# Kernel optimization log

Hardware: AMD Instinct MI355X
Metric: run time of the kernel (lower is better)

## Reference

```python
import jax, jax.numpy as jnp
import numpy as np

N, IN_DIM, HID, OUT_DIM, H = 4096, 256, 256, 256, 2
E_RAND = 131072
BN_EPS = 1e-5


def _bn(h, gamma, beta):
    # BatchNorm1d training-mode math: batch mean, biased variance
    mu = jnp.mean(h, axis=0)
    var = jnp.var(h, axis=0)
    return (h - mu) * jax.lax.rsqrt(var + BN_EPS) * gamma + beta


def setup_inputs() -> dict:
    key = jax.random.key(0)
    ks = jax.random.split(key, 16)
    x = jax.random.normal(ks[0], (N, IN_DIM), jnp.float32)
    # random edges + self loops (self loops guarantee every row has >=1 neighbor)
    rnd = jax.random.randint(ks[1], (2, E_RAND), 0, N, jnp.int64)
    loops = jnp.stack([jnp.arange(N, dtype=jnp.int64)] * 2)
    edge_index = jnp.concatenate([rnd, loops], axis=1)
    s = 1.0 / np.sqrt(IN_DIM)
    sh = 1.0 / np.sqrt(HID)
    return {
        "x": x,
        "edge_index": edge_index,
        "wq": jax.random.uniform(ks[2], (IN_DIM, HID), jnp.float32, -s, s),
        "bq": jnp.zeros((HID,), jnp.float32),
        "wk": jax.random.uniform(ks[3], (IN_DIM, HID), jnp.float32, -s, s),
        "bk": jnp.zeros((HID,), jnp.float32),
        "wv": jax.random.uniform(ks[4], (IN_DIM, HID), jnp.float32, -s, s),
        "bv": jnp.zeros((HID,), jnp.float32),
        "wo": jax.random.uniform(ks[5], (HID, IN_DIM), jnp.float32, -sh, sh),
        "bo": jnp.zeros((IN_DIM,), jnp.float32),
        "eps": jnp.zeros((1, 1), jnp.float32),
        "w1": jax.random.uniform(ks[6], (IN_DIM, HID), jnp.float32, -s, s),
        "b1": jnp.zeros((HID,), jnp.float32),
        "g1": jnp.ones((HID,), jnp.float32),
        "be1": jnp.zeros((HID,), jnp.float32),
        "w2": jax.random.uniform(ks[7], (HID, OUT_DIM), jnp.float32, -sh, sh),
        "b2": jnp.zeros((OUT_DIM,), jnp.float32),
        "g2": jnp.ones((OUT_DIM,), jnp.float32),
        "be2": jnp.zeros((OUT_DIM,), jnp.float32),
    }


def reference(x, edge_index, wq, bq, wk, bk, wv, bv, wo, bo, eps,
              w1, b1, g1, be1, w2, b2, g2, be2):
    n = x.shape[0]
    hd = HID // H
    q = (x @ wq + bq).reshape(n, H, hd)
    k = (x @ wk + bk).reshape(n, H, hd)
    v = (x @ wv + bv).reshape(n, H, hd)
    scores = jnp.einsum('nhd,mhd->nhm', q, k) / (hd ** 0.5)  # [n,H,n]
    row, col = edge_index[0], edge_index[1]
    mask = jnp.zeros((n, H, n), bool).at[row, :, col].set(True)
    scores = jnp.where(mask, scores, -jnp.inf)
    attn = jax.nn.softmax(scores, axis=-1)
    v_agg = jnp.einsum('nhm,mhd->nhd', attn, v).reshape(n, HID)
    v_agg = v_agg @ wo + bo + eps * x
    h = jax.nn.relu(_bn(v_agg @ w1 + b1, g1, be1))
    h = jax.nn.relu(_bn(h @ w2 + b2, g2, be2))
    return h  # dropout is identity (eval)
```

## Files before the change

kernel.cpp:

```cpp
#include <hip/hip_runtime.h>
#include <math.h>

#define N_NODES 4096
#define DIM 256
#define GK 256
#define MWORDS 128
#define MAXNBR 192

typedef float f32x4 __attribute__((ext_vector_type(4)));
typedef short s16x8 __attribute__((ext_vector_type(8)));
typedef short s16x4 __attribute__((ext_vector_type(4)));

__device__ __forceinline__ unsigned short bf16_rne(float f) {
  unsigned int u = __float_as_uint(f);
  u += 0x7FFFu + ((u >> 16) & 1u);
  return (unsigned short)(u >> 16);
}

__device__ __forceinline__ void split_bf16(float f, short& hi, short& lo) {
  unsigned short h = bf16_rne(f);
  float hf = __uint_as_float(((unsigned int)h) << 16);
  hi = (short)h;
  lo = (short)bf16_rne(f - hf);
}

__device__ __forceinline__ int swz(int row, int col) {
  return row * 64 + (col ^ ((row & 7) << 3));
}

template <int EPI, bool PRESPLIT, bool WRITE_C, bool SPLIT_OUT, bool STATS_OUT>
__device__ __forceinline__ void gemm_core(
    short* As_hi, short* As_lo, short* Bs_hi, short* Bs_lo, float* red,
    const float* bnsc, const float* bnsh,
    const float* __restrict__ Af, const short* __restrict__ A_hi,
    const short* __restrict__ A_lo,
    const short* __restrict__ Wt_hi, const short* __restrict__ Wt_lo,
    const float* __restrict__ bias, float* __restrict__ C, int ldc,
    short* __restrict__ C_hi, short* __restrict__ C_lo,
    int m0, int n0, const float* __restrict__ X, float ev,
    float* __restrict__ osum, float* __restrict__ osq) {
  const int tid = threadIdx.x;
  const int lane = tid & 63;
  const int wave = tid >> 6;
  const int wr = wave >> 1, wc = wave & 1;
  const int l15 = lane & 15;
  const int lg = lane >> 4;

  f32x4 acc[2][2] = {};

  for (int kt = 0; kt < GK; kt += 64) {
    __syncthreads();
    if (PRESPLIT) {
#pragma unroll
      for (int i = 0; i < 2; ++i) {
        const int row = (tid >> 3) + i * 32;
        const int kc = (tid & 7) * 8;
        const size_t g = (size_t)(m0 + row) * GK + kt + kc;
        s16x8 ah = *(const s16x8*)(A_hi + g);
        s16x8 al = *(const s16x8*)(A_lo + g);
        const int o = swz(row, kc);
        *(s16x8*)&As_hi[o] = ah;
        *(s16x8*)&As_lo[o] = al;
      }
    } else {
#pragma unroll
      for (int i = 0; i < 4; ++i) {
        const int row = (tid >> 4) + i * 16;
        const int kc = (tid & 15) * 4;
        float4 av = *(const float4*)(Af + (size_t)(m0 + row) * GK + kt + kc);
        if (EPI == 2) {
          const float4 s4 = *(const float4*)&bnsc[kt + kc];
          const float4 h4 = *(const float4*)&bnsh[kt + kc];
          av.x = fmaxf(fmaf(av.x, s4.x, h4.x), 0.f);
          av.y = fmaxf(fmaf(av.y, s4.y, h4.y), 0.f);
          av.z = fmaxf(fmaf(av.z, s4.z, h4.z), 0.f);
          av.w = fmaxf(fmaf(av.w, s4.w, h4.w), 0.f);
        }
        short h0, l0, h1, l1, h2, l2, h3, l3;
        split_bf16(av.x, h0, l0);
        split_bf16(av.y, h1, l1);
        split_bf16(av.z, h2, l2);
        split_bf16(av.w, h3, l3);
        s16x4 hv = {h0, h1, h2, h3};
        s16x4 lv = {l0, l1, l2, l3};
        const int o = swz(row, kc);
        *(s16x4*)&As_hi[o] = hv;
        *(s16x4*)&As_lo[o] = lv;
      }
    }
#pragma unroll
    for (int i = 0; i < 2; ++i) {
      const int row = (tid >> 3) + i * 32;
      const int kc = (tid & 7) * 8;
      const size_t g = (size_t)(n0 + row) * GK + kt + kc;
      s16x8 bh = *(const s16x8*)(Wt_hi + g);
      s16x8 bl = *(const s16x8*)(Wt_lo + g);
      const int o = swz(row, kc);
      *(s16x8*)&Bs_hi[o] = bh;
      *(s16x8*)&Bs_lo[o] = bl;
    }
    __syncthreads();
#pragma unroll
    for (int kk = 0; kk < 2; ++kk) {
      s16x8 ah[2], al[2], bh[2], bl[2];
#pragma unroll
      for (int f = 0; f < 2; ++f) {
        const int ao = swz(wr * 32 + f * 16 + l15, kk * 32 + lg * 8);
        const int bo = swz(wc * 32 + f * 16 + l15, kk * 32 + lg * 8);
        ah[f] = *(const s16x8*)&As_hi[ao];
        al[f] = *(const s16x8*)&As_lo[ao];
        bh[f] = *(const s16x8*)&Bs_hi[bo];
        bl[f] = *(const s16x8*)&Bs_lo[bo];
      }
#pragma unroll
      for (int fm = 0; fm < 2; ++fm)
#pragma unroll
        for (int fn = 0; fn < 2; ++fn) {
          acc[fm][fn] = __builtin_amdgcn_mfma_f32_16x16x32_bf16(ah[fm], bh[fn], acc[fm][fn], 0, 0, 0);
          acc[fm][fn] = __builtin_amdgcn_mfma_f32_16x16x32_bf16(ah[fm], bl[fn], acc[fm][fn], 0, 0, 0);
          acc[fm][fn] = __builtin_amdgcn_mfma_f32_16x16x32_bf16(al[fm], bh[fn], acc[fm][fn], 0, 0, 0);
        }
    }
  }

  float ps[2] = {0.f, 0.f}, pq[2] = {0.f, 0.f};
#pragma unroll
  for (int fm = 0; fm < 2; ++fm) {
    const int row0 = m0 + wr * 32 + fm * 16 + lg * 4;
#pragma unroll
    for (int fn = 0; fn < 2; ++fn) {
      const int col = n0 + wc * 32 + fn * 16 + l15;
      const float bb = bias[col];
#pragma unroll
      for (int j = 0; j < 4; ++j) {
        float v = acc[fm][fn][j] + bb;
        if (EPI == 1) v = fmaf(ev, X[(size_t)(row0 + j) * DIM + col], v);
        if (WRITE_C) C[(size_t)(row0 + j) * ldc + col] = v;
        if (SPLIT_OUT) {
          short hi, lo;
          split_bf16(v, hi, lo);
          C_hi[(size_t)(row0 + j) * DIM + col] = hi;
          C_lo[(size_t)(row0 + j) * DIM + col] = lo;
        }
        if (STATS_OUT) {
          ps[fn] += v;
          pq[fn] = fmaf(v, v, pq[fn]);
        }
      }
    }
  }
  if (STATS_OUT) {
    float* redS = red;
    float* redQ = red + 64;
#pragma unroll
    for (int fn = 0; fn < 2; ++fn) {
      ps[fn] += __shfl_xor(ps[fn], 16);
      ps[fn] += __shfl_xor(ps[fn], 32);
      pq[fn] += __shfl_xor(pq[fn], 16);
      pq[fn] += __shfl_xor(pq[fn], 32);
    }
    if (wr == 1 && lane < 16) {
      redS[(wc * 2 + 0) * 16 + l15] = ps[0];
      redS[(wc * 2 + 1) * 16 + l15] = ps[1];
      redQ[(wc * 2 + 0) * 16 + l15] = pq[0];
      redQ[(wc * 2 + 1) * 16 + l15] = pq[1];
    }
    __syncthreads();
    if (wr == 0 && lane < 16) {
#pragma unroll
      for (int fn = 0; fn < 2; ++fn) {
        const int col = n0 + wc * 32 + fn * 16 + l15;
        atomicAdd(&osum[col], ps[fn] + redS[(wc * 2 + fn) * 16 + l15]);
        atomicAdd(&osq[col], pq[fn] + redQ[(wc * 2 + fn) * 16 + l15]);
      }
    }
  }
}

__global__ __launch_bounds__(256) void k_prep(
    const float* __restrict__ x,
    const float* __restrict__ wq, const float* __restrict__ wk,
    const float* __restrict__ wv, const float* __restrict__ wo,
    const float* __restrict__ w1, const float* __restrict__ w2,
    const float* __restrict__ bq, const float* __restrict__ bk,
    const float* __restrict__ bv,
    unsigned int* __restrict__ mask, short* __restrict__ wt_hi,
    short* __restrict__ wt_lo, short* __restrict__ x_hi,
    short* __restrict__ x_lo, float* __restrict__ bqkv,
    float* __restrict__ stats) {
  __shared__ float tr[64][65];
  const int bid = blockIdx.x;
  const int tid = threadIdx.x;

  mask[bid * 512 + tid] = 0u;
  mask[bid * 512 + 256 + tid] = 0u;

  if (bid < 96) {
    const int mat = bid >> 4;
    const int tile = bid & 15;
    const int ti = tile >> 2;
    const int tj = tile & 3;
    const float* src = (mat == 0) ? wq : (mat == 1) ? wk : (mat == 2) ? wv
                     : (mat == 3) ? wo : (mat == 4) ? w1 : w2;
#pragma unroll
    for (int q = 0; q < 16; ++q) {
      const int r = q * 4 + (tid >> 6);
      tr[r][tid & 63] = src[(size_t)(ti * 64 + r) * 256 + tj * 64 + (tid & 63)];
    }
    __syncthreads();
    const int nbase = (mat < 3) ? mat * 256 : 768 + (mat - 3) * 256;
#pragma unroll
    for (int q = 0; q < 16; ++q) {
      const int n = q * 4 + (tid >> 6);
      const int k = tid & 63;
      short hi, lo;
      split_bf16(tr[k][n], hi, lo);
      const size_t idx = (size_t)(nbase + tj * 64 + n) * GK + ti * 64 + k;
      wt_hi[idx] = hi;
      wt_lo[idx] = lo;
    }
  } else if (bid < 608) {
    const int r0 = (bid - 96) * 8;
#pragma unroll
    for (int r = 0; r < 8; ++r) {
      const size_t g = (size_t)(r0 + r) * 256 + tid;
      short hi, lo;
      split_bf16(x[g], hi, lo);
      x_hi[g] = hi;
      x_lo[g] = lo;
    }
  } else if (bid == 608) {
    stats[tid] = 0.f;
    stats[tid + 256] = 0.f;
    stats[tid + 512] = 0.f;
    stats[tid + 768] = 0.f;
  } else if (bid >= 609 && bid < 612) {
    const int mat = bid - 609;
    bqkv[mat * 256 + tid] = (mat == 0 ? bq : mat == 1 ? bk : bv)[tid];
  }
}

__global__ __launch_bounds__(256) void k_qkv(
    const short* __restrict__ x_hi, const short* __restrict__ x_lo,
    const short* __restrict__ wt_hi, const short* __restrict__ wt_lo,
    const float* __restrict__ bqkv, float* __restrict__ qkv,
    const int* __restrict__ ei, int E, unsigned int* __restrict__ mask) {
  __shared__ __align__(16) short As_hi[4096], As_lo[4096], Bs_hi[4096], Bs_lo[4096];
  {
    const int blin = blockIdx.y * 12 + blockIdx.x;
    const int epb = (E + 767) / 768;
    const int e = blin * epb + threadIdx.x;
    if (threadIdx.x < epb && e < E) {
      const int r = ei[e];
      const int c = ei[E + e];
      atomicOr(&mask[(size_t)r * MWORDS + (c >> 5)], 1u << (c & 31));
    }
  }
  gemm_core<0, true, true, false, false>(
      As_hi, As_lo, Bs_hi, Bs_lo, nullptr, nullptr, nullptr,
      nullptr, x_hi, x_lo, wt_hi, wt_lo, bqkv, qkv, 768, nullptr, nullptr,
      blockIdx.y * 64, blockIdx.x * 64, nullptr, 0.f, nullptr, nullptr);
}

__global__ __launch_bounds__(256) void k_attn(
    const float* __restrict__ qkv, const unsigned int* __restrict__ mask,
    short* __restrict__ vagg_hi, short* __restrict__ vagg_lo) {
  __shared__ int nbr[4][MAXNBR];
  const int wave = threadIdx.x >> 6;
  const int lane = threadIdx.x & 63;
  const int r = blockIdx.x * 4 + wave;

  const unsigned int* mrow = mask + (size_t)r * MWORDS;
  int total = 0;
#pragma unroll
  for (int round = 0; round < 2; ++round) {
    unsigned int w = mrow[round * 64 + lane];
    const int cnt = __popc(w);
    int pre = cnt;
#pragma unroll
    for (int off = 1; off < 64; off <<= 1) {
      int tt = __shfl_up(pre, off);
      if (lane >= off) pre += tt;
    }
    const int wtot = __shfl(pre, 63);
    pre -= cnt;
    int base = total + pre;
    while (w) {
      const int b = __ffs(w) - 1;
      w &= w - 1;
      nbr[wave][base++] = (round * 64 + lane) * 32 + b;
    }
    total += wtot;
  }

  float4 q = *(const float4*)(qkv + (size_t)r * 768 + lane * 4);
  const float sc = 0.088388347648318447f;
  q.x *= sc; q.y *= sc; q.z *= sc; q.w *= sc;
  float4 acc = make_float4(0.f, 0.f, 0.f, 0.f);
  float m = -INFINITY, lsum = 0.f;
  const int* nb = nbr[wave];

  for (int i = 0; i < total; i += 8) {
    int cs[8];
    float4 kf[8], vf[8];
    float d[8];
#pragma unroll
    for (int j = 0; j < 8; ++j) cs[j] = (i + j < total) ? nb[i + j] : -1;
#pragma unroll
    for (int j = 0; j < 8; ++j) {
      const float* pp = qkv + (size_t)(cs[j] < 0 ? cs[0] : cs[j]) * 768 + lane * 4;
      kf[j] = *(const float4*)(pp + 256);
      vf[j] = *(const float4*)(pp + 512);
    }
#pragma unroll
    for (int j = 0; j < 8; ++j)
      d[j] = q.x * kf[j].x + q.y * kf[j].y + q.z * kf[j].z + q.w * kf[j].w;
#pragma unroll
    for (int s = 16; s >= 1; s >>= 1)
#pragma unroll
      for (int j = 0; j < 8; ++j) d[j] += __shfl_xor(d[j], s);
#pragma unroll
    for (int j = 1; j < 8; ++j)
      if (cs[j] < 0) d[j] = -INFINITY;
    float mnew = m;
#pragma unroll
    for (int j = 0; j < 8; ++j) mnew = fmaxf(mnew, d[j]);
    const float resc = __expf(m - mnew);
    float e[8], esum = 0.f;
#pragma unroll
    for (int j = 0; j < 8; ++j) {
      e[j] = __expf(d[j] - mnew);
      esum += e[j];
    }
    lsum = lsum * resc + esum;
    float ax = acc.x * resc, ay = acc.y * resc, az = acc.z * resc, aw = acc.w * resc;
#pragma unroll
    for (int j = 0; j < 8; ++j) {
      ax = fmaf(e[j], vf[j].x, ax);
      ay = fmaf(e[j], vf[j].y, ay);
      az = fmaf(e[j], vf[j].z, az);
      aw = fmaf(e[j], vf[j].w, aw);
    }
    acc.x = ax; acc.y = ay; acc.z = az; acc.w = aw;
    m = mnew;
  }
  const float inv = 1.f / lsum;
  const float o[4] = {acc.x * inv, acc.y * inv, acc.z * inv, acc.w * inv};
  short hs[4], ls[4];
#pragma unroll
  for (int j = 0; j < 4; ++j) split_bf16(o[j], hs[j], ls[j]);
  const size_t g = (size_t)r * DIM + lane * 4;
  *(s16x4*)(vagg_hi + g) = *(s16x4*)hs;
  *(s16x4*)(vagg_lo + g) = *(s16x4*)ls;
}

__global__ __launch_bounds__(256) void k_proj(
    const short* __restrict__ vagg_hi, const short* __restrict__ vagg_lo,
    const short* __restrict__ wt_hi, const short* __restrict__ wt_lo,
    const float* __restrict__ bo, const float* __restrict__ x,
    const float* __restrict__ epsp,
    short* __restrict__ a1_hi, short* __restrict__ a1_lo) {
  __shared__ __align__(16) short As_hi[4096], As_lo[4096], Bs_hi[4096], Bs_lo[4096];
  gemm_core<1, true, false, true, false>(
      As_hi, As_lo, Bs_hi, Bs_lo, nullptr, nullptr, nullptr,
      nullptr, vagg_hi, vagg_lo, wt_hi, wt_lo, bo, nullptr, DIM, a1_hi, a1_lo,
      blockIdx.y * 64, blockIdx.x * 64, x, epsp[0], nullptr, nullptr);
}

__global__ __launch_bounds__(256) void k_mlp1(
    const short* __restrict__ a1_hi, const short* __restrict__ a1_lo,
    const short* __restrict__ wt_hi, const short* __restrict__ wt_lo,
    const float* __restrict__ b1, float* __restrict__ h1,
    float* __restrict__ osum, float* __restrict__ osq) {
  __shared__ __align__(16) short As_hi[4096], As_lo[4096], Bs_hi[4096], Bs_lo[4096];
  __shared__ float red[128];
  gemm_core<0, true, true, false, true>(
      As_hi, As_lo, Bs_hi, Bs_lo, red, nullptr, nullptr,
      nullptr, a1_hi, a1_lo, wt_hi, wt_lo, b1, h1, DIM, nullptr, nullptr,
      blockIdx.y * 64, blockIdx.x * 64, nullptr, 0.f, osum, osq);
}

__global__ __launch_bounds__(256) void k_mlp2(
    const float* __restrict__ h1,
    const short* __restrict__ wt_hi, const short* __restrict__ wt_lo,
    const float* __restrict__ b2,
    const float* __restrict__ bnsum, const float* __restrict__ bnsq,
    const float* __restrict__ g1, const float* __restrict__ be1,
    float* __restrict__ h2, float* __restrict__ osum, float* __restrict__ osq) {
  __shared__ __align__(16) short As_hi[4096], As_lo[4096], Bs_hi[4096], Bs_lo[4096];
  __shared__ __align__(16) float bnsc[256], bnsh[256];
  __shared__ float red[128];
  const int tid = threadIdx.x;
  {
    const float invn = 1.f / (float)N_NODES;
    const float mu = bnsum[tid] * invn;
    const float var = bnsq[tid] * invn - mu * mu;
    const float s = g1[tid] * rsqrtf(var + 1e-5f);
    bnsc[tid] = s;
    bnsh[tid] = fmaf(-mu, s, be1[tid]);
  }
  gemm_core<2, false, true, false, true>(
      As_hi, As_lo, Bs_hi, Bs_lo, red, bnsc, bnsh,
      h1, nullptr, nullptr, wt_hi, wt_lo, b2, h2, DIM, nullptr, nullptr,
      blockIdx.y * 64, blockIdx.x * 64, nullptr, 0.f, osum, osq);
}

__global__ __launch_bounds__(256) void k_bnfinal(
    const float* __restrict__ H, const float* __restrict__ sum,
    const float* __restrict__ sumsq, const float* __restrict__ g,
    const float* __restrict__ be, float* __restrict__ out) {
  const int t = threadIdx.x;
  const int c0 = (t * 4) & (DIM - 1);
  const float invn = 1.f / (float)N_NODES;
  float4 s4 = *(const float4*)&sum[c0];
  float4 q4 = *(const float4*)&sumsq[c0];
  float4 g4 = *(const float4*)&g[c0];
  float4 b4 = *(const float4*)&be[c0];
  float scl[4], shf[4];
#pragma unroll
  for (int j = 0; j < 4; ++j) {
    const float mu = ((const float*)&s4)[j] * invn;
    const float var = ((const float*)&q4)[j] * invn - mu * mu;
    const float s = ((const float*)&g4)[j] * rsqrtf(var + 1e-5f);
    scl[j] = s;
    shf[j] = fmaf(-mu, s, ((const float*)&b4)[j]);
  }
  const int stride = gridDim.x * 256;
  for (int i = blockIdx.x * 256 + t; i < N_NODES * DIM / 4; i += stride) {
    const float4 h = ((const float4*)H)[i];
    float4 o;
    o.x = fmaxf(fmaf(h.x, scl[0], shf[0]), 0.f);
    o.y = fmaxf(fmaf(h.y, scl[1], shf[1]), 0.f);
    o.z = fmaxf(fmaf(h.z, scl[2], shf[2]), 0.f);
    o.w = fmaxf(fmaf(h.w, scl[3], shf[3]), 0.f);
    ((float4*)out)[i] = o;
  }
}

extern "C" void kernel_launch(void* const* d_in, const int* in_sizes, int n_in,
                              void* d_out, int out_size, void* d_ws, size_t ws_size,
                              hipStream_t stream) {
  const float* x   = (const float*)d_in[0];
  const int*   ei  = (const int*)d_in[1];
  const float* wq  = (const float*)d_in[2];
  const float* bq  = (const float*)d_in[3];
  const float* wk  = (const float*)d_in[4];
  const float* bk  = (const float*)d_in[5];
  const float* wv  = (const float*)d_in[6];
  const float* bv  = (const float*)d_in[7];
  const float* wo  = (const float*)d_in[8];
  const float* bo  = (const float*)d_in[9];
  const float* eps = (const float*)d_in[10];
  const float* w1  = (const float*)d_in[11];
  const float* b1  = (const float*)d_in[12];
  const float* g1  = (const float*)d_in[13];
  const float* be1 = (const float*)d_in[14];
  const float* w2  = (const float*)d_in[15];
  const float* b2  = (const float*)d_in[16];
  const float* g2  = (const float*)d_in[17];
  const float* be2 = (const float*)d_in[18];
  float* out = (float*)d_out;

  char* ws = (char*)d_ws;
  unsigned int* mask = (unsigned int*)ws;
  size_t off = (size_t)N_NODES * MWORDS * 4;
  short* wt_hi = (short*)(ws + off); off += (size_t)1536 * GK * 2;
  short* wt_lo = (short*)(ws + off); off += (size_t)1536 * GK * 2;
  short* x_hi  = (short*)(ws + off); off += (size_t)N_NODES * DIM * 2;
  short* x_lo  = (short*)(ws + off); off += (size_t)N_NODES * DIM * 2;
  short* vg_hi = (short*)(ws + off); off += (size_t)N_NODES * DIM * 2;
  short* vg_lo = (short*)(ws + off); off += (size_t)N_NODES * DIM * 2;
  short* a1_hi = (short*)(ws + off); off += (size_t)N_NODES * DIM * 2;
  short* a1_lo = (short*)(ws + off); off += (size_t)N_NODES * DIM * 2;
  float* bqkv  = (float*)(ws + off); off += 768 * 4;
  float* stats = (float*)(ws + off); off += 1024 * 4;
  off = (off + 255) & ~(size_t)255;
  float* qkv = (float*)(ws + off); off += (size_t)N_NODES * 768 * 4;
  float* h1  = (float*)(ws + off); off += (size_t)N_NODES * DIM * 4;
  float* h2  = (float*)(ws + off); off += (size_t)N_NODES * DIM * 4;

  const int E = in_sizes[1] / 2;

  k_prep<<<1024, 256, 0, stream>>>(x, wq, wk, wv, wo, w1, w2, bq, bk, bv,
                                   mask, wt_hi, wt_lo, x_hi, x_lo, bqkv, stats);
  k_qkv<<<dim3(12, 64), 256, 0, stream>>>(x_hi, x_lo, wt_hi, wt_lo, bqkv, qkv,
                                          ei, E, mask);
  k_attn<<<N_NODES / 4, 256, 0, stream>>>(qkv, mask, vg_hi, vg_lo);
  k_proj<<<dim3(4, 64), 256, 0, stream>>>(vg_hi, vg_lo,
                                          wt_hi + (size_t)768 * GK,
                                          wt_lo + (size_t)768 * GK,
                                          bo, x, eps, a1_hi, a1_lo);
  k_mlp1<<<dim3(4, 64), 256, 0, stream>>>(a1_hi, a1_lo,
                                          wt_hi + (size_t)1024 * GK,
                                          wt_lo + (size_t)1024 * GK,
                                          b1, h1, stats, stats + 256);
  k_mlp2<<<dim3(4, 64), 256, 0, stream>>>(h1,
                                          wt_hi + (size_t)1280 * GK,
                                          wt_lo + (size_t)1280 * GK,
                                          b2, stats, stats + 256, g1, be1,
                                          h2, stats + 512, stats + 768);
  k_bnfinal<<<512, 256, 0, stream>>>(h2, stats + 512, stats + 768, g2, be2, out);
}
```

Baseline: 162.3 us.

## Store K/V in bf16 for attention and halve GEMM row tiles

The QKV GEMM now writes Q as fp32 and K and V as single bf16 arrays. This halves the gather traffic in the edge-wise attention kernel, which converts K and V back to float in registers. All GEMMs also move from 64x64 tiles with a 2x2 wave layout to 32x64 tiles with each wave owning a 16-column strip, doubling the grid to fill the CUs better. The shared-memory reduction for the BN stats is dropped in favour of per-wave atomics. The risk is lower K/V precision in the attention scores and aggregation, plus more atomics and less reuse of B tiles.

```diff
diff --git a/kernel.cpp b/kernel.cpp
--- a/kernel.cpp
+++ b/kernel.cpp
@@ -17,6 +17,10 @@
   return (unsigned short)(u >> 16);
 }
 
+__device__ __forceinline__ float bf2f(unsigned short u) {
+  return __uint_as_float(((unsigned int)u) << 16);
+}
+
 __device__ __forceinline__ void split_bf16(float f, short& hi, short& lo) {
   unsigned short h = bf16_rne(f);
   float hf = __uint_as_float(((unsigned int)h) << 16);
@@ -28,64 +32,51 @@
   return row * 64 + (col ^ ((row & 7) << 3));
 }
 
-template <int EPI, bool PRESPLIT, bool WRITE_C, bool SPLIT_OUT, bool STATS_OUT>
+template <int EPI, bool PRESPLIT, int OUT, bool STATS_OUT>
 __device__ __forceinline__ void gemm_core(
-    short* As_hi, short* As_lo, short* Bs_hi, short* Bs_lo, float* red,
+    short* As_hi, short* As_lo, short* Bs_hi, short* Bs_lo,
     const float* bnsc, const float* bnsh,
     const float* __restrict__ Af, const short* __restrict__ A_hi,
     const short* __restrict__ A_lo,
     const short* __restrict__ Wt_hi, const short* __restrict__ Wt_lo,
-    const float* __restrict__ bias, float* __restrict__ C, int ldc,
-    short* __restrict__ C_hi, short* __restrict__ C_lo,
+    const float* __restrict__ bias,
+    float* __restrict__ C, short* __restrict__ C_hi, short* __restrict__ C_lo,
+    float* __restrict__ qf, unsigned short* __restrict__ kb,
+    unsigned short* __restrict__ vb,
     int m0, int n0, const float* __restrict__ X, float ev,
     float* __restrict__ osum, float* __restrict__ osq) {
   const int tid = threadIdx.x;
   const int lane = tid & 63;
-  const int wave = tid >> 6;
-  const int wr = wave >> 1, wc = wave & 1;
+  const int wc = tid >> 6;
   const int l15 = lane & 15;
   const int lg = lane >> 4;
 
-  f32x4 acc[2][2] = {};
+  f32x4 acc[2] = {};
 
   for (int kt = 0; kt < GK; kt += 64) {
     __syncthreads();
-    if (PRESPLIT) {
-#pragma unroll
-      for (int i = 0; i < 2; ++i) {
-        const int row = (tid >> 3) + i * 32;
-        const int kc = (tid & 7) * 8;
+    {
+      const int row = tid >> 3;
+      const int kc = (tid & 7) * 8;
+      if (PRESPLIT) {
         const size_t g = (size_t)(m0 + row) * GK + kt + kc;
-        s16x8 ah = *(const s16x8*)(A_hi + g);
-        s16x8 al = *(const s16x8*)(A_lo + g);
-        const int o = swz(row, kc);
-        *(s16x8*)&As_hi[o] = ah;
-        *(s16x8*)&As_lo[o] = al;
-      }
-    } else {
-#pragma unroll
-      for (int i = 0; i < 4; ++i) {
-        const int row = (tid >> 4) + i * 16;
-        const int kc = (tid & 15) * 4;
-        float4 av = *(const float4*)(Af + (size_t)(m0 + row) * GK + kt + kc);
+        *(s16x8*)&As_hi[swz(row, kc)] = *(const s16x8*)(A_hi + g);
+        *(s16x8*)&As_lo[swz(row, kc)] = *(const s16x8*)(A_lo + g);
+      } else {
+        const float* src = Af + (size_t)(m0 + row) * GK + kt + kc;
+        float a[8];
+        *(float4*)&a[0] = *(const float4*)src;
+        *(float4*)&a[4] = *(const float4*)(src + 4);
         if (EPI == 2) {
-          const float4 s4 = *(const float4*)&bnsc[kt + kc];
-          const float4 h4 = *(const float4*)&bnsh[kt + kc];
-          av.x = fmaxf(fmaf(av.x, s4.x, h4.x), 0.f);
-          av.y = fmaxf(fmaf(av.y, s4.y, h4.y), 0.f);
-          av.z = fmaxf(fmaf(av.z, s4.z, h4.z), 0.f);
-          av.w = fmaxf(fmaf(av.w, s4.w, h4.w), 0.f);
+#pragma unroll
+          for (int i = 0; i < 8; ++i)
+            a[i] = fmaxf(fmaf(a[i], bnsc[kt + kc + i], bnsh[kt + kc + i]), 0.f);
         }
-        short h0, l0, h1, l1, h2, l2, h3, l3;
-        split_bf16(av.x, h0, l0);
-        split_bf16(av.y, h1, l1);
-        split_bf16(av.z, h2, l2);
-        split_bf16(av.w, h3, l3);
-        s16x4 hv = {h0, h1, h2, h3};
-        s16x4 lv = {l0, l1, l2, l3};
-        const int o = swz(row, kc);
-        *(s16x4*)&As_hi[o] = hv;
-        *(s16x4*)&As_lo[o] = lv;
+        short h[8], l[8];
+#pragma unroll
+        for (int i = 0; i < 8; ++i) split_bf16(a[i], h[i], l[i]);
+        *(s16x8*)&As_hi[swz(row, kc)] = *(const s16x8*)h;
+        *(s16x8*)&As_lo[swz(row, kc)] = *(const s16x8*)l;
       }
     }
 #pragma unroll
@@ -93,86 +84,68 @@
       const int row = (tid >> 3) + i * 32;
       const int kc = (tid & 7) * 8;
       const size_t g = (size_t)(n0 + row) * GK + kt + kc;
-      s16x8 bh = *(const s16x8*)(Wt_hi + g);
-      s16x8 bl = *(const s16x8*)(Wt_lo + g);
-      const int o = swz(row, kc);
-      *(s16x8*)&Bs_hi[o] = bh;
-      *(s16x8*)&Bs_lo[o] = bl;
+      *(s16x8*)&Bs_hi[swz(row, kc)] = *(const s16x8*)(Wt_hi + g);
+      *(s16x8*)&Bs_lo[swz(row, kc)] = *(const s16x8*)(Wt_lo + g);
     }
     __syncthreads();
 #pragma unroll
     for (int kk = 0; kk < 2; ++kk) {
-      s16x8 ah[2], al[2], bh[2], bl[2];
+      s16x8 ah[2], al[2];
 #pragma unroll
       for (int f = 0; f < 2; ++f) {
-        const int ao = swz(wr * 32 + f * 16 + l15, kk * 32 + lg * 8);
-        const int bo = swz(wc * 32 + f * 16 + l15, kk * 32 + lg * 8);
+        const int ao = swz(f * 16 + l15, kk * 32 + lg * 8);
         ah[f] = *(const s16x8*)&As_hi[ao];
         al[f] = *(const s16x8*)&As_lo[ao];
-        bh[f] = *(const s16x8*)&Bs_hi[bo];
-        bl[f] = *(const s16x8*)&Bs_lo[bo];
-      }
-#pragma unroll
-      for (int fm = 0; fm < 2; ++fm)
-#pragma unroll
-        for (int fn = 0; fn < 2; ++fn) {
-          acc[fm][fn] = __builtin_amdgcn_mfma_f32_16x16x32_bf16(ah[fm], bh[fn], acc[fm][fn], 0, 0, 0);
-          acc[fm][fn] = __builtin_amdgcn_mfma_f32_16x16x32_bf16(ah[fm], bl[fn], acc[fm][fn], 0, 0, 0);
-          acc[fm][fn] = __builtin_amdgcn_mfma_f32_16x16x32_bf16(al[fm], bh[fn], acc[fm][fn], 0, 0, 0);
-        }
-    }
-  }
-
-  float ps[2] = {0.f, 0.f}, pq[2] = {0.f, 0.f};
+      }
+      const int bo_ = swz(wc * 16 + l15, kk * 32 + lg * 8);
+      const s16x8 bh = *(const s16x8*)&Bs_hi[bo_];
+      const s16x8 bl = *(const s16x8*)&Bs_lo[bo_];
+#pragma unroll
+      for (int f = 0; f < 2; ++f) {
+        acc[f] = __builtin_amdgcn_mfma_f32_16x16x32_bf16(ah[f], bh, acc[f], 0, 0, 0);
+        acc[f] = __builtin_amdgcn_mfma_f32_16x16x32_bf16(ah[f], bl, acc[f], 0, 0, 0);
+        acc[f] = __builtin_amdgcn_mfma_f32_16x16x32_bf16(al[f], bh, acc[f], 0, 0, 0);
+      }
+    }
+  }
+
+  const int col = n0 + wc * 16 + l15;
+  const float bb = bias[col];
+  float ps = 0.f, pq = 0.f;
 #pragma unroll
   for (int fm = 0; fm < 2; ++fm) {
-    const int row0 = m0 + wr * 32 + fm * 16 + lg * 4;
-#pragma unroll
-    for (int fn = 0; fn < 2; ++fn) {
-      const int col = n0 + wc * 32 + fn * 16 + l15;
-      const float bb = bias[col];
-#pragma unroll
-      for (int j = 0; j < 4; ++j) {
-        float v = acc[fm][fn][j] + bb;
-        if (EPI == 1) v = fmaf(ev, X[(size_t)(row0 + j) * DIM + col], v);
-        if (WRITE_C) C[(size_t)(row0 + j) * ldc + col] = v;
-        if (SPLIT_OUT) {
-          short hi, lo;
-          split_bf16(v, hi, lo);
-          C_hi[(size_t)(row0 + j) * DIM + col] = hi;
-          C_lo[(size_t)(row0 + j) * DIM + col] = lo;
-        }
-        if (STATS_OUT) {
-          ps[fn] += v;
-          pq[fn] = fmaf(v, v, pq[fn]);
-        }
+    const int row0 = m0 + fm * 16 + lg * 4;
+#pragma unroll
+    for (int j = 0; j < 4; ++j) {
+      const int row = row0 + j;
+      float v = acc[fm][j] + bb;
+      if (EPI == 1) v = fmaf(ev, X[(size_t)row * DIM + col], v);
+      if (OUT == 0) C[(size_t)row * DIM + col] = v;
+      if (OUT == 1) {
+        short hi, lo;
+        split_bf16(v, hi, lo);
+        C_hi[(size_t)row * DIM + col] = hi;
+        C_lo[(size_t)row * DIM + col] = lo;
+      }
+      if (OUT == 2) {
+        if (n0 < 256) qf[(size_t)row * DIM + col] = v;
+        else if (n0 < 512) kb[(size_t)row * DIM + col - 256] = bf16_rne(v);
+        else vb[(size_t)row * DIM + col - 512] = bf16_rne(v);
+      }
+      if (STATS_OUT) {
+        ps += v;
+        pq = fmaf(v, v, pq);
       }
     }
   }
   if (STATS_OUT) {
-    float* redS = red;
-    float* redQ = red + 64;
-#pragma unroll
-    for (int fn = 0; fn < 2; ++fn) {
-      ps[fn] += __shfl_xor(ps[fn], 16);
-      ps[fn] += __shfl_xor(ps[fn], 32);
-      pq[fn] += __shfl_xor(pq[fn], 16);
-      pq[fn] += __shfl_xor(pq[fn], 32);
-    }
-    if (wr == 1 && lane < 16) {
-      redS[(wc * 2 + 0) * 16 + l15] = ps[0];
-      redS[(wc * 2 + 1) * 16 + l15] = ps[1];
-      redQ[(wc * 2 + 0) * 16 + l15] = pq[0];
-      redQ[(wc * 2 + 1) * 16 + l15] = pq[1];
-    }
-    __syncthreads();
-    if (wr == 0 && lane < 16) {
-#pragma unroll
-      for (int fn = 0; fn < 2; ++fn) {
-        const int col = n0 + wc * 32 + fn * 16 + l15;
-        atomicAdd(&osum[col], ps[fn] + redS[(wc * 2 + fn) * 16 + l15]);
-        atomicAdd(&osq[col], pq[fn] + redQ[(wc * 2 + fn) * 16 + l15]);
-      }
+    ps += __shfl_xor(ps, 16);
+    ps += __shfl_xor(ps, 32);
+    pq += __shfl_xor(pq, 16);
+    pq += __shfl_xor(pq, 32);
+    if (lane < 16) {
+      atomicAdd(&osum[col], ps);
+      atomicAdd(&osq[col], pq);
     }
   }
 }
@@ -243,12 +216,13 @@
 __global__ __launch_bounds__(256) void k_qkv(
     const short* __restrict__ x_hi, const short* __restrict__ x_lo,
     const short* __restrict__ wt_hi, const short* __restrict__ wt_lo,
-    const float* __restrict__ bqkv, float* __restrict__ qkv,
+    const float* __restrict__ bqkv, float* __restrict__ qf,
+    unsigned short* __restrict__ kb, unsigned short* __restrict__ vb,
     const int* __restrict__ ei, int E, unsigned int* __restrict__ mask) {
-  __shared__ __align__(16) short As_hi[4096], As_lo[4096], Bs_hi[4096], Bs_lo[4096];
+  __shared__ __align__(16) short As_hi[2048], As_lo[2048], Bs_hi[4096], Bs_lo[4096];
   {
     const int blin = blockIdx.y * 12 + blockIdx.x;
-    const int epb = (E + 767) / 768;
+    const int epb = (E + 1535) / 1536;
     const int e = blin * epb + threadIdx.x;
     if (threadIdx.x < epb && e < E) {
       const int r = ei[e];
@@ -256,14 +230,16 @@
       atomicOr(&mask[(size_t)r * MWORDS + (c >> 5)], 1u << (c & 31));
     }
   }
-  gemm_core<0, true, true, false, false>(
-      As_hi, As_lo, Bs_hi, Bs_lo, nullptr, nullptr, nullptr,
-      nullptr, x_hi, x_lo, wt_hi, wt_lo, bqkv, qkv, 768, nullptr, nullptr,
-      blockIdx.y * 64, blockIdx.x * 64, nullptr, 0.f, nullptr, nullptr);
+  gemm_core<0, true, 2, false>(
+      As_hi, As_lo, Bs_hi, Bs_lo, nullptr, nullptr,
+      nullptr, x_hi, x_lo, wt_hi, wt_lo, bqkv,
+      nullptr, nullptr, nullptr, qf, kb, vb,
+      blockIdx.y * 32, blockIdx.x * 64, nullptr, 0.f, nullptr, nullptr);
 }
 
 __global__ __launch_bounds__(256) void k_attn(
-    const float* __restrict__ qkv, const unsigned int* __restrict__ mask,
+    const float* __restrict__ qf, const unsigned short* __restrict__ kb,
+    const unsigned short* __restrict__ vb, const unsigned int* __restrict__ mask,
     short* __restrict__ vagg_hi, short* __restrict__ vagg_lo) {
   __shared__ int nbr[4][MAXNBR];
   const int wave = threadIdx.x >> 6;
@@ -293,7 +269,7 @@
     total += wtot;
   }
 
-  float4 q = *(const float4*)(qkv + (size_t)r * 768 + lane * 4);
+  float4 q = *(const float4*)(qf + (size_t)r * DIM + lane * 4);
   const float sc = 0.088388347648318447f;
   q.x *= sc; q.y *= sc; q.z *= sc; q.w *= sc;
   float4 acc = make_float4(0.f, 0.f, 0.f, 0.f);
@@ -302,19 +278,20 @@
 
   for (int i = 0; i < total; i += 8) {
     int cs[8];
-    float4 kf[8], vf[8];
+    ushort4 ku[8], vu[8];
     float d[8];
 #pragma unroll
     for (int j = 0; j < 8; ++j) cs[j] = (i + j < total) ? nb[i + j] : -1;
 #pragma unroll
     for (int j = 0; j < 8; ++j) {
-      const float* pp = qkv + (size_t)(cs[j] < 0 ? cs[0] : cs[j]) * 768 + lane * 4;
-      kf[j] = *(const float4*)(pp + 256);
-      vf[j] = *(const float4*)(pp + 512);
+      const size_t g = (size_t)(cs[j] < 0 ? cs[0] : cs[j]) * DIM + lane * 4;
+      ku[j] = *(const ushort4*)(kb + g);
+      vu[j] = *(const ushort4*)(vb + g);
     }
 #pragma unroll
     for (int j = 0; j < 8; ++j)
-      d[j] = q.x * kf[j].x + q.y * kf[j].y + q.z * kf[j].z + q.w * kf[j].w;
+      d[j] = q.x * bf2f(ku[j].x) + q.y * bf2f(ku[j].y) +
+             q.z * bf2f(ku[j].z) + q.w * bf2f(ku[j].w);
 #pragma unroll
     for (int s = 16; s >= 1; s >>= 1)
 #pragma unroll
@@ -336,10 +313,10 @@
     float ax = acc.x * resc, ay = acc.y * resc, az = acc.z * resc, aw = acc.w * resc;
 #pragma unroll
     for (int j = 0; j < 8; ++j) {
-      ax = fmaf(e[j], vf[j].x, ax);
-      ay = fmaf(e[j], vf[j].y, ay);
-      az = fmaf(e[j], vf[j].z, az);
-      aw = fmaf(e[j], vf[j].w, aw);
+      ax = fmaf(e[j], bf2f(vu[j].x), ax);
+      ay = fmaf(e[j], bf2f(vu[j].y), ay);
+      az = fmaf(e[j], bf2f(vu[j].z), az);
+      aw = fmaf(e[j], bf2f(vu[j].w), aw);
     }
     acc.x = ax; acc.y = ay; acc.z = az; acc.w = aw;
     m = mnew;
@@ -360,11 +337,12 @@
     const float* __restrict__ bo, const float* __restrict__ x,
     const float* __restrict__ epsp,
     short* __restrict__ a1_hi, short* __restrict__ a1_lo) {
-  __shared__ __align__(16) short As_hi[4096], As_lo[4096], Bs_hi[4096], Bs_lo[4096];
-  gemm_core<1, true, false, true, false>(
-      As_hi, As_lo, Bs_hi, Bs_lo, nullptr, nullptr, nullptr,
-      nullptr, vagg_hi, vagg_lo, wt_hi, wt_lo, bo, nullptr, DIM, a1_hi, a1_lo,
-      blockIdx.y * 64, blockIdx.x * 64, x, epsp[0], nullptr, nullptr);
+  __shared__ __align__(16) short As_hi[2048], As_lo[2048], Bs_hi[4096], Bs_lo[4096];
+  gemm_core<1, true, 1, false>(
+      As_hi, As_lo, Bs_hi, Bs_lo, nullptr, nullptr,
+      nullptr, vagg_hi, vagg_lo, wt_hi, wt_lo, bo,
+      nullptr, a1_hi, a1_lo, nullptr, nullptr, nullptr,
+      blockIdx.y * 32, blockIdx.x * 64, x, epsp[0], nullptr, nullptr);
 }
 
 __global__ __launch_bounds__(256) void k_mlp1(
@@ -372,12 +350,12 @@
     const short* __restrict__ wt_hi, const short* __restrict__ wt_lo,
     const float* __restrict__ b1, float* __restrict__ h1,
     float* __restrict__ osum, float* __restrict__ osq) {
-  __shared__ __align__(16) short As_hi[4096], As_lo[4096], Bs_hi[4096], Bs_lo[4096];
-  __shared__ float red[128];
-  gemm_core<0, true, true, false, true>(
-      As_hi, As_lo, Bs_hi, Bs_lo, red, nullptr, nullptr,
-      nullptr, a1_hi, a1_lo, wt_hi, wt_lo, b1, h1, DIM, nullptr, nullptr,
-      blockIdx.y * 64, blockIdx.x * 64, nullptr, 0.f, osum, osq);
+  __shared__ __align__(16) short As_hi[2048], As_lo[2048], Bs_hi[4096], Bs_lo[4096];
+  gemm_core<0, true, 0, true>(
+      As_hi, As_lo, Bs_hi, Bs_lo, nullptr, nullptr,
+      nullptr, a1_hi, a1_lo, wt_hi, wt_lo, b1,
+      h1, nullptr, nullptr, nullptr, nullptr, nullptr,
+      blockIdx.y * 32, blockIdx.x * 64, nullptr, 0.f, osum, osq);
 }
 
 __global__ __launch_bounds__(256) void k_mlp2(
@@ -387,9 +365,8 @@
     const float* __restrict__ bnsum, const float* __restrict__ bnsq,
     const float* __restrict__ g1, const float* __restrict__ be1,
     float* __restrict__ h2, float* __restrict__ osum, float* __restrict__ osq) {
-  __shared__ __align__(16) short As_hi[4096], As_lo[4096], Bs_hi[4096], Bs_lo[4096];
+  __shared__ __align__(16) short As_hi[2048], As_lo[2048], Bs_hi[4096], Bs_lo[4096];
   __shared__ __align__(16) float bnsc[256], bnsh[256];
-  __shared__ float red[128];
   const int tid = threadIdx.x;
   {
     const float invn = 1.f / (float)N_NODES;
@@ -399,10 +376,11 @@
     bnsc[tid] = s;
     bnsh[tid] = fmaf(-mu, s, be1[tid]);
   }
-  gemm_core<2, false, true, false, true>(
-      As_hi, As_lo, Bs_hi, Bs_lo, red, bnsc, bnsh,
-      h1, nullptr, nullptr, wt_hi, wt_lo, b2, h2, DIM, nullptr, nullptr,
-      blockIdx.y * 64, blockIdx.x * 64, nullptr, 0.f, osum, osq);
+  gemm_core<2, false, 0, true>(
+      As_hi, As_lo, Bs_hi, Bs_lo, bnsc, bnsh,
+      h1, nullptr, nullptr, wt_hi, wt_lo, b2,
+      h2, nullptr, nullptr, nullptr, nullptr, nullptr,
+      blockIdx.y * 32, blockIdx.x * 64, nullptr, 0.f, osum, osq);
 }
 
 __global__ __launch_bounds__(256) void k_bnfinal(
@@ -472,32 +450,34 @@
   short* vg_lo = (short*)(ws + off); off += (size_t)N_NODES * DIM * 2;
   short* a1_hi = (short*)(ws + off); off += (size_t)N_NODES * DIM * 2;
   short* a1_lo = (short*)(ws + off); off += (size_t)N_NODES * DIM * 2;
+  unsigned short* kb = (unsigned short*)(ws + off); off += (size_t)N_NODES * DIM * 2;
+  unsigned short* vb = (unsigned short*)(ws + off); off += (size_t)N_NODES * DIM * 2;
   float* bqkv  = (float*)(ws + off); off += 768 * 4;
   float* stats = (float*)(ws + off); off += 1024 * 4;
   off = (off + 255) & ~(size_t)255;
-  float* qkv = (float*)(ws + off); off += (size_t)N_NODES * 768 * 4;
-  float* h1  = (float*)(ws + off); off += (size_t)N_NODES * DIM * 4;
-  float* h2  = (float*)(ws + off); off += (size_t)N_NODES * DIM * 4;
+  float* qf = (float*)(ws + off); off += (size_t)N_NODES * DIM * 4;
+  float* h1 = (float*)(ws + off); off += (size_t)N_NODES * DIM * 4;
+  float* h2 = (float*)(ws + off); off += (size_t)N_NODES * DIM * 4;
 
   const int E = in_sizes[1] / 2;
 
   k_prep<<<1024, 256, 0, stream>>>(x, wq, wk, wv, wo, w1, w2, bq, bk, bv,
                                    mask, wt_hi, wt_lo, x_hi, x_lo, bqkv, stats);
-  k_qkv<<<dim3(12, 64), 256, 0, stream>>>(x_hi, x_lo, wt_hi, wt_lo, bqkv, qkv,
-                                          ei, E, mask);
-  k_attn<<<N_NODES / 4, 256, 0, stream>>>(qkv, mask, vg_hi, vg_lo);
-  k_proj<<<dim3(4, 64), 256, 0, stream>>>(vg_hi, vg_lo,
-                                          wt_hi + (size_t)768 * GK,
-                                          wt_lo + (size_t)768 * GK,
-                                          bo, x, eps, a1_hi, a1_lo);
-  k_mlp1<<<dim3(4, 64), 256, 0, stream>>>(a1_hi, a1_lo,
-                                          wt_hi + (size_t)1024 * GK,
-                                          wt_lo + (size_t)1024 * GK,
-                                          b1, h1, stats, stats + 256);
-  k_mlp2<<<dim3(4, 64), 256, 0, stream>>>(h1,
-                                          wt_hi + (size_t)1280 * GK,
-                                          wt_lo + (size_t)1280 * GK,
-                                          b2, stats, stats + 256, g1, be1,
-                                          h2, stats + 512, stats + 768);
+  k_qkv<<<dim3(12, 128), 256, 0, stream>>>(x_hi, x_lo, wt_hi, wt_lo, bqkv,
+                                           qf, kb, vb, ei, E, mask);
+  k_attn<<<N_NODES / 4, 256, 0, stream>>>(qf, kb, vb, mask, vg_hi, vg_lo);
+  k_proj<<<dim3(4, 128), 256, 0, stream>>>(vg_hi, vg_lo,
+                                           wt_hi + (size_t)768 * GK,
+                                           wt_lo + (size_t)768 * GK,
+                                           bo, x, eps, a1_hi, a1_lo);
+  k_mlp1<<<dim3(4, 128), 256, 0, stream>>>(a1_hi, a1_lo,
+                                           wt_hi + (size_t)1024 * GK,
+                                           wt_lo + (size_t)1024 * GK,
+                                           b1, h1, stats, stats + 256);
+  k_mlp2<<<dim3(4, 128), 256, 0, stream>>>(h1,
+                                           wt_hi + (size_t)1280 * GK,
+                                           wt_lo + (size_t)1280 * GK,
+                                           b2, stats, stats + 256, g1, be1,
+                                           h2, stats + 512, stats + 768);
   k_bnfinal<<<512, 256, 0, stream>>>(h2, stats + 512, stats + 768, g2, be2, out);
 }
```

Measured after the change: 158.9 us. 2.1% less time.
